# Kernel optimization log

Measured on AMD Instinct MI355X. Metric: run time of the kernel, lower is better.

## Reference

```python
import jax, jax.numpy as jnp
import numpy as np
from jax import lax

H = W = 128            # feature map spatial size (2h x 2w)
WIN = 16               # attention window size
DIM = 512
HEADS = 8
DIM_HEAD = 64
INNER = HEADS * DIM_HEAD
SCALE = DIM_HEAD ** -0.5
KEEP = 44
IOU_T = 0.2

_s = np.arange(0, H - WIN + 1, WIN // 2)
_sx, _sy = np.meshgrid(_s, _s)
WINDOWS = np.stack([_sx.ravel(), _sy.ravel(), _sx.ravel() + WIN - 1, _sy.ravel() + WIN - 1], 1).astype(np.float32)
M = WINDOWS.shape[0]   # 225
SX = jnp.asarray(WINDOWS[:, 0].astype(np.int32))
SY = jnp.asarray(WINDOWS[:, 1].astype(np.int32))

# ---- static pairwise IoU (torchvision convention: area=(x2-x1)*(y2-y1)) ----
_x1, _y1, _x2, _y2 = WINDOWS[:, 0], WINDOWS[:, 1], WINDOWS[:, 2], WINDOWS[:, 3]
_area = (_x2 - _x1) * (_y2 - _y1)
_iw = np.clip(np.minimum(_x2[:, None], _x2[None]) - np.maximum(_x1[:, None], _x1[None]), 0, None)
_ih = np.clip(np.minimum(_y2[:, None], _y2[None]) - np.maximum(_y1[:, None], _y1[None]), 0, None)
_inter = _iw * _ih
IOU = jnp.asarray((_inter / (_area[:, None] + _area[None] - _inter)).astype(np.float32))

# ---- roi_align (aligned=False, 1 sample/bin) == separable bilinear resample ----
_bin = (WIN - 1.0) / WIN
_r = (np.arange(WIN) + 0.5) * _bin
_q = np.floor(_r).astype(int)
_f = _r - _q
_A = np.zeros((WIN, WIN), np.float32)
_A[np.arange(WIN), _q] = 1.0 - _f
_A[np.arange(WIN), np.minimum(_q + 1, WIN - 1)] += _f
BILIN = jnp.asarray(_A)


def _nms_select(score):
    """Greedy NMS over the static window set; return first KEEP kept indices."""
    order = jnp.argsort(-score)
    iou_s = IOU[order][:, order]
    def body(i, supp):
        return supp | ((~supp[i]) & (iou_s[i] > IOU_T) & (jnp.arange(M) > i))
    supp = lax.fori_loop(0, M, body, jnp.zeros((M,), dtype=bool))
    pos = jnp.where(~supp, jnp.arange(M), M)
    pos = jnp.minimum(jnp.sort(pos)[:KEEP], M - 1)
    return order[pos]


def setup_inputs() -> dict:
    key = jax.random.key(0)
    k1, k2, k3, k4 = jax.random.split(key, 4)
    x = jax.random.normal(k1, (8, H * W, DIM), dtype=jnp.float32)
    prob = jax.random.uniform(k2, (8, 4, H // 2, W // 2), dtype=jnp.float32)
    W_fix = jnp.ones((1, 1, WIN // 2, WIN // 2), jnp.float32)   # FixCNN ones kernel
    W_qkv = jax.random.normal(k3, (3 * INNER, DIM), jnp.float32) * 0.02
    W_out = jax.random.normal(k4, (DIM, INNER), jnp.float32) * 0.02
    b_out = jnp.zeros((DIM,), jnp.float32)
    return {"x": x, "prob": prob, "W_fix": W_fix, "W_qkv": W_qkv, "W_out": W_out, "b_out": b_out}


def reference(x, prob, W_fix, W_qkv, W_out, b_out):
    b = x.shape[0]
    # entropy over class channels
    entropy = -jnp.sum(prob * jnp.log2(prob + 1e-10), axis=1)           # (b, 64, 64)
    # FixCNN: ones 8x8 kernel, stride 4, then /64
    score = lax.conv(entropy[:, None], W_fix, (WIN // 4, WIN // 4), 'VALID')
    score = (score / float((WIN // 2) ** 2)).reshape(b, -1)             # (b, M)
    x2d = x.transpose(0, 2, 1).reshape(b, DIM, H, W)                    # b d h w
    rng = jnp.arange(WIN)

    def per_batch(feat, sc):
        idx = _nms_select(sc)                                           # (KEEP,)
        sy, sx = SY[idx], SX[idx]
        # gather integer 16x16 patches (box corners are integers)
        patches = jax.vmap(lambda y, xc: lax.dynamic_slice(feat, (0, y, xc), (DIM, WIN, WIN)))(sy, sx)
        # roi_align bilinear resample (separable)
        pat = jnp.einsum('pi,mdij,qj->mdpq', BILIN, patches, BILIN)     # (KEEP, d, 16, 16)
        xi = pat.transpose(0, 2, 3, 1).reshape(KEEP, WIN * WIN, DIM)    # m n d
        qkv = xi @ W_qkv.T
        q, k, v = jnp.split(qkv, 3, axis=-1)
        to_h = lambda t: t.reshape(KEEP, WIN * WIN, HEADS, DIM_HEAD).transpose(0, 2, 1, 3)
        q, k, v = to_h(q), to_h(k), to_h(v)
        attn = jax.nn.softmax(jnp.einsum('mhnd,mhkd->mhnk', q, k) * SCALE, axis=-1)
        out = jnp.einsum('mhnk,mhkd->mhnd', attn, v)
        out = out.transpose(0, 2, 1, 3).reshape(KEEP, WIN * WIN, INNER)
        out = out @ W_out.T + b_out                                     # (KEEP, n, DIM)
        out2d = out.reshape(KEEP, WIN, WIN, DIM).transpose(0, 3, 1, 2)  # m d h w
        yy = sy[:, None, None] + rng[None, :, None]                     # (KEEP,16,1)
        xx = sx[:, None, None] + rng[None, None, :]                     # (KEEP,1,16)
        acc = jnp.zeros((DIM, H, W), x.dtype).at[:, yy, xx].add(out2d.transpose(1, 0, 2, 3))
        cnt = jnp.zeros((H, W), x.dtype).at[yy, xx].add(1.0)
        return acc, cnt

    acc, cnt = jax.vmap(per_batch)(x2d, score)
    outx = (acc / (cnt[:, None] + 1e-10)).reshape(b, DIM, H * W).transpose(0, 2, 1)
    return x + outx
```

## Files before the change

kernel.cpp:

```cpp
#include <hip/hip_runtime.h>
#include <type_traits>
#include <utility>

typedef unsigned short u16;
typedef __attribute__((ext_vector_type(8))) short short8;
typedef __attribute__((ext_vector_type(8))) __bf16 bf16v8;
typedef __attribute__((ext_vector_type(4))) float f32x4;

template <typename T, typename = void> struct mfma_ok : std::false_type {};
template <typename T>
struct mfma_ok<T, std::void_t<decltype(__builtin_amdgcn_mfma_f32_16x16x32_bf16(
    std::declval<T>(), std::declval<T>(), std::declval<f32x4>(), 0, 0, 0))>>
    : std::true_type {};
using frag8 = std::conditional_t<mfma_ok<bf16v8>::value, bf16v8, short8>;

#define MFMA16(a, b, c) __builtin_amdgcn_mfma_f32_16x16x32_bf16((a), (b), (c), 0, 0, 0)

__device__ __forceinline__ float bf2f(u16 u) {
  unsigned v = ((unsigned)u) << 16;
  return __builtin_bit_cast(float, v);
}
__device__ __forceinline__ u16 f2bf(float f) {
  unsigned u = __builtin_bit_cast(unsigned, f);
  u = (u + 0x7fffu + ((u >> 16) & 1u)) >> 16;
  return (u16)u;
}
__device__ __forceinline__ unsigned cvtpk_bf16(float lo, float hi) {
  unsigned r;
  asm("v_cvt_pk_bf16_f32 %0, %1, %2" : "=v"(r) : "v"(lo), "v"(hi));
  return r;
}
__device__ __forceinline__ void gl16(const u16* g, u16* l) {
  __builtin_amdgcn_global_load_lds((__attribute__((address_space(1))) void*)(g),
                                   (__attribute__((address_space(3))) void*)(l), 16, 0, 0);
}

__global__ void k_score(const float* __restrict__ prob, const float* __restrict__ wfix,
                        float* __restrict__ scores) {
  const int b = blockIdx.x, tid = threadIdx.x;
  __shared__ float ent[64 * 64];
  __shared__ float wf[64];
  if (tid < 64) wf[tid] = wfix[tid];
  const float* pb = prob + (size_t)b * 4 * 4096;
  for (int p = tid; p < 4096; p += 256) {
    float e = 0.f;
#pragma unroll
    for (int ch = 0; ch < 4; ++ch) {
      float v = pb[ch * 4096 + p];
      e -= v * log2f(v + 1e-10f);
    }
    ent[p] = e;
  }
  __syncthreads();
  if (tid < 225) {
    int wy = tid / 15, wx = tid % 15;
    float s = 0.f;
    for (int a = 0; a < 8; ++a)
      for (int c = 0; c < 8; ++c)
        s += ent[(wy * 4 + a) * 64 + wx * 4 + c] * wf[a * 8 + c];
    scores[b * 225 + tid] = s * (1.0f / 64.0f);
  }
}

__device__ __forceinline__ float iou_pair(int wa, int wb) {
  float x1a = (float)((wa % 15) * 8), y1a = (float)((wa / 15) * 8);
  float x1b = (float)((wb % 15) * 8), y1b = (float)((wb / 15) * 8);
  float iw = fminf(x1a, x1b) + 15.f - fmaxf(x1a, x1b);
  float ih = fminf(y1a, y1b) + 15.f - fmaxf(y1a, y1b);
  iw = fmaxf(iw, 0.f);
  ih = fmaxf(ih, 0.f);
  float inter = iw * ih;
  return inter / (450.f - inter);
}

__global__ void k_nms(const float* __restrict__ scores, int* __restrict__ sel,
                      int* __restrict__ kept, float* __restrict__ mult) {
  const int b = blockIdx.x, t = threadIdx.x;
  __shared__ float s[225];
  __shared__ int order[225];
  __shared__ unsigned char supp[225];
  __shared__ int idx44[44];
  __shared__ int ks[225];
  __shared__ float ml[225];
  if (t < 225) s[t] = scores[b * 225 + t];
  __syncthreads();
  if (t < 225) {
    float st = s[t];
    int r = 0;
    for (int j = 0; j < 225; ++j) {
      float sj = s[j];
      r += (sj > st) || (sj == st && j < t);
    }
    order[r] = t;
    supp[t] = 0;
    ks[t] = -1;
    ml[t] = 0.f;
  }
  __syncthreads();
  for (int i = 0; i < 224; ++i) {
    if (t > i && t < 225 && !supp[i]) {
      if (iou_pair(order[i], order[t]) > 0.2f) supp[t] = 1;
    }
    __syncthreads();
  }
  if (t == 0) {
    int k = 0;
    for (int i = 0; i < 225 && k < 44; ++i)
      if (!supp[i]) idx44[k++] = order[i];
    while (k < 44) idx44[k++] = order[224];
    for (int k2 = 0; k2 < 44; ++k2) {
      int w = idx44[k2];
      if (ks[w] < 0) ks[w] = k2;
      ml[w] += 1.f;
    }
  }
  __syncthreads();
  if (t < 225) {
    kept[b * 225 + t] = ks[t];
    mult[b * 225 + t] = ml[t];
  }
  if (t < 44) sel[b * 44 + t] = idx44[t];
}

__global__ void k_castw(const float* __restrict__ Wq, const float* __restrict__ Wo,
                        u16* __restrict__ wqb, u16* __restrict__ wob) {
  int idx = blockIdx.x * 256 + threadIdx.x;
  if (idx < 786432) wqb[idx] = f2bf(Wq[idx]);
  int i2 = idx - 786432;
  if (i2 >= 0 && i2 < 262144) wob[i2] = f2bf(Wo[i2]);
}

__global__ __launch_bounds__(256) void k_gather(const float* __restrict__ x,
                                                const int* __restrict__ sel,
                                                u16* __restrict__ xi) {
  const size_t idx = (size_t)blockIdx.x * 256 + threadIdx.x;
  const int dc = (int)(idx & 63);
  const int pq = (int)((idx >> 6) & 255);
  const int g = (int)(idx >> 14);
  const int b = g / 44;
  const int w = sel[g];
  const int sy = (w / 15) * 8, sx = (w % 15) * 8;
  const int p = pq >> 4, q = pq & 15;
  float rp = ((float)p + 0.5f) * 0.9375f;
  int i0 = (int)rp;
  float fp = rp - (float)i0;
  float rq = ((float)q + 0.5f) * 0.9375f;
  int j0 = (int)rq;
  float fq = rq - (float)j0;
  const float w00 = (1.f - fp) * (1.f - fq), w01 = (1.f - fp) * fq;
  const float w10 = fp * (1.f - fq), w11 = fp * fq;
  const float* xb = x + ((size_t)b * 16384 + (size_t)(sy + i0) * 128 + sx + j0) * 512 + dc * 8;
  const float4* t00 = (const float4*)xb;
  const float4* t01 = (const float4*)(xb + 512);
  const float4* t10 = (const float4*)(xb + 512 * 128);
  const float4* t11 = (const float4*)(xb + 512 * 129);
  float acc[8];
#pragma unroll
  for (int h = 0; h < 2; ++h) {
    float4 a = t00[h], bb = t01[h], c = t10[h], d = t11[h];
    acc[h * 4 + 0] = w00 * a.x + w01 * bb.x + w10 * c.x + w11 * d.x;
    acc[h * 4 + 1] = w00 * a.y + w01 * bb.y + w10 * c.y + w11 * d.y;
    acc[h * 4 + 2] = w00 * a.z + w01 * bb.z + w10 * c.z + w11 * d.z;
    acc[h * 4 + 3] = w00 * a.w + w01 * bb.w + w10 * c.w + w11 * d.w;
  }
  short8 o;
#pragma unroll
  for (int e = 0; e < 8; ++e) o[e] = (short)f2bf(acc[e]);
  *(short8*)&xi[((size_t)g * 256 + pq) * 512 + dc * 8] = o;
}

template <int BIAS>
__global__ __launch_bounds__(256) void k_gemm(const u16* __restrict__ A, const u16* __restrict__ B,
                                              u16* __restrict__ C, const float* __restrict__ bias,
                                              int M, int N, int K) {
  __shared__ u16 sA[128 * 32];
  __shared__ u16 sB[128 * 32];
  const int tid = threadIdx.x, lane = tid & 63, wv = tid >> 6;
  const int bn = blockIdx.x, bm = blockIdx.y;
  const int wm = (wv >> 1) * 64, wn = (wv & 1) * 64;
  const int lb0 = wv * 2048, lb1 = wv * 2048 + 1024;
  const int gb0 = lb0 + lane * 16, gb1 = lb1 + lane * 16;
  const int r0 = gb0 >> 6, c0 = (gb0 & 63) >> 1;
  const int r1 = gb1 >> 6, c1 = (gb1 & 63) >> 1;
  const u16* Ag0 = A + (size_t)(bm * 128 + r0) * K + c0;
  const u16* Ag1 = A + (size_t)(bm * 128 + r1) * K + c1;
  const u16* Bg0 = B + (size_t)(bn * 128 + r0) * K + c0;
  const u16* Bg1 = B + (size_t)(bn * 128 + r1) * K + c1;
  u16* lA0 = &sA[lb0 >> 1];
  u16* lA1 = &sA[lb1 >> 1];
  u16* lB0 = &sB[lb0 >> 1];
  u16* lB1 = &sB[lb1 >> 1];
  f32x4 acc[4][4] = {};
  const int ra = wm + (lane & 15), rb = wn + (lane & 15), k8 = (lane >> 4) * 8;
  for (int kt = 0; kt < K; kt += 32) {
    gl16(Ag0 + kt, lA0);
    gl16(Ag1 + kt, lA1);
    gl16(Bg0 + kt, lB0);
    gl16(Bg1 + kt, lB1);
    __syncthreads();
    frag8 af[4], bf[4];
#pragma unroll
    for (int i = 0; i < 4; ++i) af[i] = *(const frag8*)&sA[(ra + i * 16) * 32 + k8];
#pragma unroll
    for (int i = 0; i < 4; ++i) bf[i] = *(const frag8*)&sB[(rb + i * 16) * 32 + k8];
#pragma unroll
    for (int i = 0; i < 4; ++i)
#pragma unroll
      for (int j = 0; j < 4; ++j) acc[i][j] = MFMA16(af[i], bf[j], acc[i][j]);
    __syncthreads();
  }
  const int cc = lane & 15, rr = (lane >> 4) * 4;
#pragma unroll
  for (int i = 0; i < 4; ++i)
#pragma unroll
    for (int j = 0; j < 4; ++j)
#pragma unroll
      for (int e = 0; e < 4; ++e) {
        int row = bm * 128 + wm + i * 16 + rr + e;
        int col = bn * 128 + wn + j * 16 + cc;
        float v = acc[i][j][e];
        if (BIAS) v += bias[col];
        C[(size_t)row * N + col] = f2bf(v);
      }
}

__global__ __launch_bounds__(256, 2) void k_attn(const u16* __restrict__ qkv,
                                                 u16* __restrict__ aout) {
  const int g = blockIdx.x;
  const int win = g >> 3, h = g & 7;
  const int tid = threadIdx.x, lane = tid & 63, wv = tid >> 6;
  __shared__ u16 Kb[2][64][68];
  __shared__ u16 Vt[64][258];
  __shared__ u16 Ps[4][64][36];
  const u16* base = qkv + (size_t)win * 256 * 1536;
  const u16* kbase = base + 512 + h * 64;
  const u16* vbase = base + 1024 + h * 64;
  const int prow = tid >> 2, pc16 = (tid & 3) * 16;

  {
    const u16* kp = kbase + (size_t)prow * 1536 + pc16;
    short8 a = *(const short8*)kp;
    short8 b2 = *(const short8*)(kp + 8);
    *(short8*)&Kb[0][prow][pc16] = a;
    *(short8*)&Kb[0][prow][pc16 + 8] = b2;
  }
  {
    const u16* vp = vbase + (size_t)tid * 1536;
#pragma unroll
    for (int c8 = 0; c8 < 64; c8 += 8) {
      short8 v = *(const short8*)(vp + c8);
#pragma unroll
      for (int e2 = 0; e2 < 8; ++e2) Vt[c8 + e2][tid] = (u16)v[e2];
    }
  }
  frag8 qf[4][2];
#pragma unroll
  for (int mf = 0; mf < 4; ++mf)
#pragma unroll
    for (int kk = 0; kk < 2; ++kk)
      qf[mf][kk] = *(const frag8*)(base + (size_t)(wv * 64 + mf * 16 + (lane & 15)) * 1536 +
                                   h * 64 + kk * 32 + (lane >> 4) * 8);
  __syncthreads();

  float m_run[4][4], l_run[4][4];
  f32x4 of[4][4];
#pragma unroll
  for (int mf = 0; mf < 4; ++mf)
#pragma unroll
    for (int j = 0; j < 4; ++j) {
      m_run[mf][j] = -3e38f;
      l_run[mf][j] = 0.f;
    }
#pragma unroll
  for (int mf = 0; mf < 4; ++mf)
#pragma unroll
    for (int df = 0; df < 4; ++df) of[mf][df] = 0.f;

  u16(*Pw)[36] = Ps[wv];
  int cur = 0;
  for (int kb = 0; kb < 4; ++kb) {
    short8 pf0 = {}, pf1 = {};
    if (kb < 3) {
      const u16* kp = kbase + (size_t)((kb + 1) * 64 + prow) * 1536 + pc16;
      pf0 = *(const short8*)kp;
      pf1 = *(const short8*)(kp + 8);
    }
    f32x4 sf[4][4] = {};
#pragma unroll
    for (int kk = 0; kk < 2; ++kk) {
      frag8 kf[4];
#pragma unroll
      for (int nf = 0; nf < 4; ++nf)
        kf[nf] = *(const frag8*)&Kb[cur][nf * 16 + (lane & 15)][kk * 32 + (lane >> 4) * 8];
#pragma unroll
      for (int mf = 0; mf < 4; ++mf)
#pragma unroll
        for (int nf = 0; nf < 4; ++nf) sf[mf][nf] = MFMA16(qf[mf][kk], kf[nf], sf[mf][nf]);
    }
#pragma unroll
    for (int mf = 0; mf < 4; ++mf) {
#pragma unroll
      for (int j = 0; j < 4; ++j) {
        float bm = fmaxf(fmaxf(sf[mf][0][j], sf[mf][1][j]), fmaxf(sf[mf][2][j], sf[mf][3][j]));
        bm = fmaxf(bm, __shfl_xor(bm, 1));
        bm = fmaxf(bm, __shfl_xor(bm, 2));
        bm = fmaxf(bm, __shfl_xor(bm, 4));
        bm = fmaxf(bm, __shfl_xor(bm, 8));
        float mo = m_run[mf][j];
        float mn = fmaxf(mo, bm);
        float corr = __expf((mo - mn) * 0.125f);
        m_run[mf][j] = mn;
        float ls = 0.f;
#pragma unroll
        for (int nf = 0; nf < 4; ++nf) {
          float p = __expf((sf[mf][nf][j] - mn) * 0.125f);
          sf[mf][nf][j] = p;
          ls += p;
        }
        l_run[mf][j] = l_run[mf][j] * corr + ls;
#pragma unroll
        for (int df = 0; df < 4; ++df) of[mf][df][j] *= corr;
      }
    }
#pragma unroll
    for (int kk = 0; kk < 2; ++kk) {
#pragma unroll
      for (int mf = 0; mf < 4; ++mf)
#pragma unroll
        for (int nl = 0; nl < 2; ++nl) {
          int nf = kk * 2 + nl;
          int rr0 = mf * 16 + (lane >> 4) * 4;
          int c = nl * 16 + (lane & 15);
          unsigned p01 = cvtpk_bf16(sf[mf][nf][0], sf[mf][nf][1]);
          unsigned p23 = cvtpk_bf16(sf[mf][nf][2], sf[mf][nf][3]);
          Pw[rr0][c] = (u16)p01;
          Pw[rr0 + 1][c] = (u16)(p01 >> 16);
          Pw[rr0 + 2][c] = (u16)p23;
          Pw[rr0 + 3][c] = (u16)(p23 >> 16);
        }
      asm volatile("" ::: "memory");
      frag8 pa[4], vb[4];
#pragma unroll
      for (int mf = 0; mf < 4; ++mf)
        pa[mf] = *(const frag8*)&Pw[mf * 16 + (lane & 15)][(lane >> 4) * 8];
#pragma unroll
      for (int df = 0; df < 4; ++df)
        vb[df] = *(const frag8*)&Vt[df * 16 + (lane & 15)][kb * 64 + kk * 32 + (lane >> 4) * 8];
#pragma unroll
      for (int mf = 0; mf < 4; ++mf)
#pragma unroll
        for (int df = 0; df < 4; ++df) of[mf][df] = MFMA16(pa[mf], vb[df], of[mf][df]);
      asm volatile("" ::: "memory");
    }
    if (kb < 3) {
      *(short8*)&Kb[cur ^ 1][prow][pc16] = pf0;
      *(short8*)&Kb[cur ^ 1][prow][pc16 + 8] = pf1;
    }
    __syncthreads();
    cur ^= 1;
  }
#pragma unroll
  for (int mf = 0; mf < 4; ++mf)
#pragma unroll
    for (int j = 0; j < 4; ++j) {
      float lt = l_run[mf][j];
      lt += __shfl_xor(lt, 1);
      lt += __shfl_xor(lt, 2);
      lt += __shfl_xor(lt, 4);
      lt += __shfl_xor(lt, 8);
      float inv = 1.0f / lt;
#pragma unroll
      for (int df = 0; df < 4; ++df) {
        int row = win * 256 + wv * 64 + mf * 16 + (lane >> 4) * 4 + j;
        int col = h * 64 + df * 16 + (lane & 15);
        aout[(size_t)row * 512 + col] = f2bf(of[mf][df][j] * inv);
      }
    }
}

__global__ void k_final(const float* __restrict__ x, const u16* __restrict__ proj,
                        const int* __restrict__ kept, const float* __restrict__ mult,
                        float* __restrict__ out) {
  const size_t idx = (size_t)blockIdx.x * 256 + threadIdx.x;
  const int dci = (int)(idx & 31);
  const int pix = (int)((idx >> 5) & 16383);
  const int b = (int)(idx >> 19);
  const int y = pix >> 7, xc = pix & 127;
  float acc[16];
#pragma unroll
  for (int e = 0; e < 16; ++e) acc[e] = 0.f;
  float c = 0.f;
  const int wyh = y >> 3, wxh = xc >> 3;
#pragma unroll
  for (int a = 0; a < 2; ++a) {
    int wy = wyh - 1 + a;
    if (wy < 0 || wy > 14) continue;
#pragma unroll
    for (int bb = 0; bb < 2; ++bb) {
      int wx = wxh - 1 + bb;
      if (wx < 0 || wx > 14) continue;
      int w = wy * 15 + wx;
      int slot = kept[b * 225 + w];
      if (slot < 0) continue;
      float ml = mult[b * 225 + w];
      c += ml;
      const u16* pr = proj +
                      ((size_t)((b * 44 + slot) * 256 + (y - wy * 8) * 16 + (xc - wx * 8))) * 512 +
                      (size_t)dci * 16;
      short8 v0 = *(const short8*)pr;
      short8 v1 = *(const short8*)(pr + 8);
#pragma unroll
      for (int e = 0; e < 8; ++e) acc[e] += ml * bf2f((u16)v0[e]);
#pragma unroll
      for (int e = 0; e < 8; ++e) acc[8 + e] += ml * bf2f((u16)v1[e]);
    }
  }
  const float inv = 1.f / (c + 1e-10f);
  const size_t off = ((size_t)(b * 16384 + pix)) * 512 + (size_t)dci * 16;
  const float4* xp = (const float4*)(x + off);
  float4* op = (float4*)(out + off);
#pragma unroll
  for (int q4 = 0; q4 < 4; ++q4) {
    float4 xv = xp[q4];
    float4 ov;
    ov.x = xv.x + acc[q4 * 4 + 0] * inv;
    ov.y = xv.y + acc[q4 * 4 + 1] * inv;
    ov.z = xv.z + acc[q4 * 4 + 2] * inv;
    ov.w = xv.w + acc[q4 * 4 + 3] * inv;
    op[q4] = ov;
  }
}

extern "C" void kernel_launch(void* const* d_in, const int* in_sizes, int n_in, void* d_out,
                              int out_size, void* d_ws, size_t ws_size, hipStream_t stream) {
  const float* x = (const float*)d_in[0];
  const float* prob = (const float*)d_in[1];
  const float* wfix = (const float*)d_in[2];
  const float* Wq = (const float*)d_in[3];
  const float* Wo = (const float*)d_in[4];
  const float* bo = (const float*)d_in[5];
  float* out = (float*)d_out;
  char* ws = (char*)d_ws;

  float* scores = (float*)(ws + 0);
  int* sel = (int*)(ws + 8192);
  int* kept = (int*)(ws + 16384);
  float* mult = (float*)(ws + 24576);
  u16* wqb = (u16*)(ws + 32768);
  u16* wob = (u16*)(ws + 32768 + 1572864);
  u16* xi = (u16*)(ws + 4194304);
  u16* qkv = (u16*)(ws + 4194304 + 92274688);
  u16* aout = xi;
  u16* proj = qkv;

  k_score<<<8, 256, 0, stream>>>(prob, wfix, scores);
  k_nms<<<8, 256, 0, stream>>>(scores, sel, kept, mult);
  k_castw<<<4096, 256, 0, stream>>>(Wq, Wo, wqb, wob);
  k_gather<<<22528, 256, 0, stream>>>(x, sel, xi);
  k_gemm<0><<<dim3(12, 704), 256, 0, stream>>>(xi, wqb, qkv, nullptr, 90112, 1536, 512);
  k_attn<<<2816, 256, 0, stream>>>(qkv, aout);
  k_gemm<1><<<dim3(4, 704), 256, 0, stream>>>(aout, wob, proj, bo, 90112, 512, 512);
  k_final<<<16384, 256, 0, stream>>>(x, proj, kept, mult, out);
}
```

Before: 789.0 us.

## Rewrite window attention with 32x32 MFMA, transposed scores, and register-resident P

The attention kernel now computes S^T = K·Q^T with 32x32x16 bf16 MFMAs, so each lane holds one query column. Row max and sum reductions then need a single cross-half shuffle instead of four xor shuffles. P is repacked into MFMA B-operands through lane-32 shuffles instead of a round trip through per-wave LDS. It also adds a lazy rescale that skips the correction unless the max grows beyond a threshold, and stages the output through LDS for 16-byte coalesced global stores. This cuts LDS traffic and shuffle overhead, at the cost of more complex lane bookkeeping and a shared LDS buffer reused for output staging.

```diff
diff --git a/kernel.cpp b/kernel.cpp
--- a/kernel.cpp
+++ b/kernel.cpp
@@ -6,6 +6,7 @@
 typedef __attribute__((ext_vector_type(8))) short short8;
 typedef __attribute__((ext_vector_type(8))) __bf16 bf16v8;
 typedef __attribute__((ext_vector_type(4))) float f32x4;
+typedef __attribute__((ext_vector_type(16))) float f32x16;
 
 template <typename T, typename = void> struct mfma_ok : std::false_type {};
 template <typename T>
@@ -15,6 +16,7 @@
 using frag8 = std::conditional_t<mfma_ok<bf16v8>::value, bf16v8, short8>;
 
 #define MFMA16(a, b, c) __builtin_amdgcn_mfma_f32_16x16x32_bf16((a), (b), (c), 0, 0, 0)
+#define MFMA32(a, b, c) __builtin_amdgcn_mfma_f32_32x32x16_bf16((a), (b), (c), 0, 0, 0)
 
 __device__ __forceinline__ float bf2f(u16 u) {
   unsigned v = ((unsigned)u) << 16;
@@ -229,9 +231,11 @@
   const int g = blockIdx.x;
   const int win = g >> 3, h = g & 7;
   const int tid = threadIdx.x, lane = tid & 63, wv = tid >> 6;
-  __shared__ u16 Kb[2][64][68];
-  __shared__ u16 Vt[64][258];
-  __shared__ u16 Ps[4][64][36];
+  const int l31 = lane & 31, l5 = lane >> 5;
+  const bool lo32 = (lane < 32);
+  __shared__ u16 smem[25344];
+  u16* KbB = smem;
+  u16* VtB = smem + 8704;
   const u16* base = qkv + (size_t)win * 256 * 1536;
   const u16* kbase = base + 512 + h * 64;
   const u16* vbase = base + 1024 + h * 64;
@@ -239,10 +243,8 @@
 
   {
     const u16* kp = kbase + (size_t)prow * 1536 + pc16;
-    short8 a = *(const short8*)kp;
-    short8 b2 = *(const short8*)(kp + 8);
-    *(short8*)&Kb[0][prow][pc16] = a;
-    *(short8*)&Kb[0][prow][pc16 + 8] = b2;
+    *(short8*)&KbB[prow * 68 + pc16] = *(const short8*)kp;
+    *(short8*)&KbB[prow * 68 + pc16 + 8] = *(const short8*)(kp + 8);
   }
   {
     const u16* vp = vbase + (size_t)tid * 1536;
@@ -250,33 +252,22 @@
     for (int c8 = 0; c8 < 64; c8 += 8) {
       short8 v = *(const short8*)(vp + c8);
 #pragma unroll
-      for (int e2 = 0; e2 < 8; ++e2) Vt[c8 + e2][tid] = (u16)v[e2];
-    }
-  }
-  frag8 qf[4][2];
-#pragma unroll
-  for (int mf = 0; mf < 4; ++mf)
-#pragma unroll
-    for (int kk = 0; kk < 2; ++kk)
-      qf[mf][kk] = *(const frag8*)(base + (size_t)(wv * 64 + mf * 16 + (lane & 15)) * 1536 +
-                                   h * 64 + kk * 32 + (lane >> 4) * 8);
-  __syncthreads();
-
-  float m_run[4][4], l_run[4][4];
-  f32x4 of[4][4];
-#pragma unroll
-  for (int mf = 0; mf < 4; ++mf)
-#pragma unroll
-    for (int j = 0; j < 4; ++j) {
-      m_run[mf][j] = -3e38f;
-      l_run[mf][j] = 0.f;
-    }
-#pragma unroll
-  for (int mf = 0; mf < 4; ++mf)
-#pragma unroll
-    for (int df = 0; df < 4; ++df) of[mf][df] = 0.f;
-
-  u16(*Pw)[36] = Ps[wv];
+      for (int e2 = 0; e2 < 8; ++e2) VtB[(c8 + e2) * 260 + tid] = (u16)v[e2];
+    }
+  }
+  frag8 qf[2][4];
+#pragma unroll
+  for (int qt = 0; qt < 2; ++qt)
+#pragma unroll
+    for (int c = 0; c < 4; ++c)
+      qf[qt][c] = *(const frag8*)(base + (size_t)(wv * 64 + qt * 32 + l31) * 1536 + h * 64 +
+                                  c * 16 + l5 * 8);
+  __syncthreads();
+
+  f32x16 of[2][2] = {};
+  float m_run[2] = {-3e38f, -3e38f};
+  float l_run[2] = {0.f, 0.f};
+
   int cur = 0;
   for (int kb = 0; kb < 4; ++kb) {
     short8 pf0 = {}, pf1 = {};
@@ -285,97 +276,109 @@
       pf0 = *(const short8*)kp;
       pf1 = *(const short8*)(kp + 8);
     }
-    f32x4 sf[4][4] = {};
-#pragma unroll
-    for (int kk = 0; kk < 2; ++kk) {
-      frag8 kf[4];
-#pragma unroll
-      for (int nf = 0; nf < 4; ++nf)
-        kf[nf] = *(const frag8*)&Kb[cur][nf * 16 + (lane & 15)][kk * 32 + (lane >> 4) * 8];
-#pragma unroll
-      for (int mf = 0; mf < 4; ++mf)
-#pragma unroll
-        for (int nf = 0; nf < 4; ++nf) sf[mf][nf] = MFMA16(qf[mf][kk], kf[nf], sf[mf][nf]);
-    }
-#pragma unroll
-    for (int mf = 0; mf < 4; ++mf) {
-#pragma unroll
-      for (int j = 0; j < 4; ++j) {
-        float bm = fmaxf(fmaxf(sf[mf][0][j], sf[mf][1][j]), fmaxf(sf[mf][2][j], sf[mf][3][j]));
-        bm = fmaxf(bm, __shfl_xor(bm, 1));
-        bm = fmaxf(bm, __shfl_xor(bm, 2));
-        bm = fmaxf(bm, __shfl_xor(bm, 4));
-        bm = fmaxf(bm, __shfl_xor(bm, 8));
-        float mo = m_run[mf][j];
-        float mn = fmaxf(mo, bm);
-        float corr = __expf((mo - mn) * 0.125f);
-        m_run[mf][j] = mn;
-        float ls = 0.f;
-#pragma unroll
-        for (int nf = 0; nf < 4; ++nf) {
-          float p = __expf((sf[mf][nf][j] - mn) * 0.125f);
-          sf[mf][nf][j] = p;
-          ls += p;
+#pragma unroll
+    for (int qt = 0; qt < 2; ++qt) {
+      f32x16 s0 = {}, s1 = {};
+#pragma unroll
+      for (int c = 0; c < 4; ++c) {
+        frag8 kf0 = *(const frag8*)&KbB[cur * 4352 + l31 * 68 + c * 16 + l5 * 8];
+        frag8 kf1 = *(const frag8*)&KbB[cur * 4352 + (32 + l31) * 68 + c * 16 + l5 * 8];
+        s0 = MFMA32(kf0, qf[qt][c], s0);
+        s1 = MFMA32(kf1, qf[qt][c], s1);
+      }
+      float tm[16];
+#pragma unroll
+      for (int r = 0; r < 16; ++r) tm[r] = fmaxf(s0[r], s1[r]);
+#pragma unroll
+      for (int r = 0; r < 8; ++r) tm[r] = fmaxf(tm[r], tm[r + 8]);
+#pragma unroll
+      for (int r = 0; r < 4; ++r) tm[r] = fmaxf(tm[r], tm[r + 4]);
+      float pm = fmaxf(fmaxf(tm[0], tm[1]), fmaxf(tm[2], tm[3]));
+      pm = fmaxf(pm, __shfl_xor(pm, 32));
+      if (!__all(pm <= m_run[qt] + 64.f)) {
+        float mn = fmaxf(m_run[qt], pm);
+        float corr = __expf((m_run[qt] - mn) * 0.125f);
+        l_run[qt] *= corr;
+#pragma unroll
+        for (int dt = 0; dt < 2; ++dt)
+#pragma unroll
+          for (int r = 0; r < 16; ++r) of[qt][dt][r] *= corr;
+        m_run[qt] = mn;
+      }
+      const float mqt = m_run[qt];
+      float ls = 0.f;
+#pragma unroll
+      for (int kt = 0; kt < 2; ++kt) {
+        const f32x16 sv = kt ? s1 : s0;
+        float p[16];
+#pragma unroll
+        for (int r = 0; r < 16; ++r) p[r] = __expf((sv[r] - mqt) * 0.125f);
+        float e0 = (p[0] + p[1]) + (p[2] + p[3]);
+        float e1 = (p[4] + p[5]) + (p[6] + p[7]);
+        float e2 = (p[8] + p[9]) + (p[10] + p[11]);
+        float e3 = (p[12] + p[13]) + (p[14] + p[15]);
+        ls += (e0 + e1) + (e2 + e3);
+#pragma unroll
+        for (int cc = 0; cc < 2; ++cc) {
+          const int bx = cc * 8;
+          unsigned a0 = cvtpk_bf16(p[bx + 0], p[bx + 1]);
+          unsigned a1 = cvtpk_bf16(p[bx + 2], p[bx + 3]);
+          unsigned b0 = cvtpk_bf16(p[bx + 4], p[bx + 5]);
+          unsigned b1 = cvtpk_bf16(p[bx + 6], p[bx + 7]);
+          unsigned sa0 = __shfl_xor(a0, 32);
+          unsigned sa1 = __shfl_xor(a1, 32);
+          unsigned sb0 = __shfl_xor(b0, 32);
+          unsigned sb1 = __shfl_xor(b1, 32);
+          uint4 fu;
+          fu.x = lo32 ? a0 : sb0;
+          fu.y = lo32 ? a1 : sb1;
+          fu.z = lo32 ? sa0 : b0;
+          fu.w = lo32 ? sa1 : b1;
+          frag8 pb = __builtin_bit_cast(frag8, fu);
+#pragma unroll
+          for (int dt = 0; dt < 2; ++dt) {
+            frag8 va = *(const frag8*)&VtB[(dt * 32 + l31) * 260 + kb * 64 + kt * 32 + cc * 16 +
+                                           l5 * 8];
+            of[qt][dt] = MFMA32(va, pb, of[qt][dt]);
+          }
         }
-        l_run[mf][j] = l_run[mf][j] * corr + ls;
-#pragma unroll
-        for (int df = 0; df < 4; ++df) of[mf][df][j] *= corr;
       }
-    }
-#pragma unroll
-    for (int kk = 0; kk < 2; ++kk) {
-#pragma unroll
-      for (int mf = 0; mf < 4; ++mf)
-#pragma unroll
-        for (int nl = 0; nl < 2; ++nl) {
-          int nf = kk * 2 + nl;
-          int rr0 = mf * 16 + (lane >> 4) * 4;
-          int c = nl * 16 + (lane & 15);
-          unsigned p01 = cvtpk_bf16(sf[mf][nf][0], sf[mf][nf][1]);
-          unsigned p23 = cvtpk_bf16(sf[mf][nf][2], sf[mf][nf][3]);
-          Pw[rr0][c] = (u16)p01;
-          Pw[rr0 + 1][c] = (u16)(p01 >> 16);
-          Pw[rr0 + 2][c] = (u16)p23;
-          Pw[rr0 + 3][c] = (u16)(p23 >> 16);
-        }
-      asm volatile("" ::: "memory");
-      frag8 pa[4], vb[4];
-#pragma unroll
-      for (int mf = 0; mf < 4; ++mf)
-        pa[mf] = *(const frag8*)&Pw[mf * 16 + (lane & 15)][(lane >> 4) * 8];
-#pragma unroll
-      for (int df = 0; df < 4; ++df)
-        vb[df] = *(const frag8*)&Vt[df * 16 + (lane & 15)][kb * 64 + kk * 32 + (lane >> 4) * 8];
-#pragma unroll
-      for (int mf = 0; mf < 4; ++mf)
-#pragma unroll
-        for (int df = 0; df < 4; ++df) of[mf][df] = MFMA16(pa[mf], vb[df], of[mf][df]);
-      asm volatile("" ::: "memory");
+      l_run[qt] += ls;
     }
     if (kb < 3) {
-      *(short8*)&Kb[cur ^ 1][prow][pc16] = pf0;
-      *(short8*)&Kb[cur ^ 1][prow][pc16 + 8] = pf1;
+      *(short8*)&KbB[(cur ^ 1) * 4352 + prow * 68 + pc16] = pf0;
+      *(short8*)&KbB[(cur ^ 1) * 4352 + prow * 68 + pc16 + 8] = pf1;
     }
     __syncthreads();
     cur ^= 1;
   }
-#pragma unroll
-  for (int mf = 0; mf < 4; ++mf)
-#pragma unroll
-    for (int j = 0; j < 4; ++j) {
-      float lt = l_run[mf][j];
-      lt += __shfl_xor(lt, 1);
-      lt += __shfl_xor(lt, 2);
-      lt += __shfl_xor(lt, 4);
-      lt += __shfl_xor(lt, 8);
-      float inv = 1.0f / lt;
-#pragma unroll
-      for (int df = 0; df < 4; ++df) {
-        int row = win * 256 + wv * 64 + mf * 16 + (lane >> 4) * 4 + j;
-        int col = h * 64 + df * 16 + (lane & 15);
-        aout[(size_t)row * 512 + col] = f2bf(of[mf][df][j] * inv);
+
+  float inv[2];
+#pragma unroll
+  for (int qt = 0; qt < 2; ++qt) {
+    float lt = l_run[qt] + __shfl_xor(l_run[qt], 32);
+    inv[qt] = 1.0f / lt;
+  }
+  u16* sc = smem + wv * 4352;
+#pragma unroll
+  for (int qt = 0; qt < 2; ++qt)
+#pragma unroll
+    for (int dt = 0; dt < 2; ++dt)
+#pragma unroll
+      for (int j = 0; j < 4; ++j) {
+        unsigned w0 = cvtpk_bf16(of[qt][dt][4 * j + 0] * inv[qt], of[qt][dt][4 * j + 1] * inv[qt]);
+        unsigned w1 = cvtpk_bf16(of[qt][dt][4 * j + 2] * inv[qt], of[qt][dt][4 * j + 3] * inv[qt]);
+        *(uint2*)&sc[(qt * 32 + l31) * 68 + dt * 32 + 8 * j + 4 * l5] = make_uint2(w0, w1);
       }
-    }
+  __syncthreads();
+#pragma unroll
+  for (int rep = 0; rep < 8; ++rep) {
+    int row = rep * 8 + (lane >> 3);
+    uint2 lo = *(const uint2*)&sc[row * 68 + (lane & 7) * 8];
+    uint2 hi = *(const uint2*)&sc[row * 68 + (lane & 7) * 8 + 4];
+    *(int4*)&aout[(size_t)(win * 256 + wv * 64 + row) * 512 + h * 64 + (lane & 7) * 8] =
+        make_int4((int)lo.x, (int)lo.y, (int)hi.x, (int)hi.y);
+  }
 }
 
 __global__ void k_final(const float* __restrict__ x, const u16* __restrict__ proj,
```

Result: faster. 766.5 us (-2.8%).
